# Kernel optimization log

Hardware: AMD Instinct MI355X
Metric: run time of the kernel (lower is better)

The kernel has to match this reference:

```python
import jax, jax.numpy as jnp
import numpy as np

START_ID = 1  # id of the start symbol in the vocabulary


def setup_inputs() -> dict:
    key = jax.random.key(0)
    ks = jax.random.split(key, 11)
    B, T, V, E, H, F = 64, 32, 10000, 300, 256, 4096
    s = 0.05
    return {
        "X": jax.random.normal(ks[0], (B, F), jnp.float32),
        "emb_table": jax.random.normal(ks[1], (V, E), jnp.float32),
        "fc1_w": jax.random.normal(ks[2], (H, F), jnp.float32) * s,
        "fc1_b": jax.random.normal(ks[3], (H,), jnp.float32) * s,
        "w_ih": jax.random.normal(ks[4], (4 * H, H + E), jnp.float32) * s,
        "w_hh": jax.random.normal(ks[5], (4 * H, H), jnp.float32) * s,
        "b_ih": jax.random.normal(ks[6], (4 * H,), jnp.float32) * s,
        "b_hh": jax.random.normal(ks[7], (4 * H,), jnp.float32) * s,
        "fc2_w": jax.random.normal(ks[8], (V, H), jnp.float32) * s,
        "fc2_b": jax.random.normal(ks[9], (V,), jnp.float32) * s,
        "label": jax.random.randint(ks[10], (T, B), 0, V, jnp.int64),
        "max_sentence_len": T,
    }


def reference(X, emb_table, fc1_w, fc1_b, w_ih, w_hh, b_ih, b_hh, fc2_w, fc2_b,
              label, max_sentence_len):
    T = max_sentence_len
    B = X.shape[0]
    V, H = fc2_w.shape
    E = emb_table.shape[1]

    # fc1: project image features to hidden size
    Xp = X @ fc1_w.T + fc1_b  # [B, H]

    # word embedding input per step: step 1 uses start symbol,
    # step idx>=2 uses teacher-forced embedding of label[idx-1]
    start_emb = jnp.broadcast_to(emb_table[START_ID], (1, B, E))
    tf_emb = emb_table[label[1:T - 1]]          # [T-2, B, E]
    embeds = jnp.concatenate([start_emb, tf_emb], axis=0)  # [T-1, B, E]

    h0 = jnp.zeros((B, H), X.dtype)
    c0 = jnp.zeros((B, H), X.dtype)

    def step(carry, e):
        h, c = carry
        x = jnp.concatenate([Xp, e], axis=1)  # [B, H+E]
        gates = x @ w_ih.T + b_ih + h @ w_hh.T + b_hh  # [B, 4H]
        i, f, g, o = jnp.split(gates, 4, axis=1)
        i = jax.nn.sigmoid(i)
        f = jax.nn.sigmoid(f)
        g = jnp.tanh(g)
        o = jax.nn.sigmoid(o)
        c = f * c + i * g
        h = o * jnp.tanh(c)
        logp = jax.nn.log_softmax(h @ fc2_w.T + fc2_b, axis=-1)  # [B, V]
        return (h, c), logp

    _, probs = jax.lax.scan(step, (h0, c0), embeds)  # [T-1, B, V]

    # first timestep: one-hot of the start word (as in the torch code)
    start_onehot = jnp.zeros((1, B, V), X.dtype).at[:, :, START_ID].set(1.0)
    result = jnp.concatenate([start_onehot, probs], axis=0)  # [T, B, V]
    return jnp.transpose(result, (1, 0, 2))  # [B, T, V]
```

## Files before the change

### kernel.cpp

```cpp
#include <hip/hip_runtime.h>
#include <hip/hip_bf16.h>
#include <math.h>

#define B_   64
#define T_   32
#define S_   31
#define V_   10000
#define E_   300
#define H_   256
#define F_   4096
#define G4   1024
#define HE   556
#define MPAD 2048
#define NPAD 10112
#define START_ID 1
#define NBL  4

#define FP0 10112
#define FP1 (FP0 + 128)
#define FP2 (FP1 + 2500)
#define FP3 (FP2 + 512)
#define FP4 (FP3 + 300)

typedef __bf16 bf16x8 __attribute__((ext_vector_type(8)));
typedef float  f32x4  __attribute__((ext_vector_type(4)));

__device__ __forceinline__ float bf16bits_to_f(unsigned int u) {
    union { unsigned int i; float f; } c; c.i = u; return c.f;
}
__device__ __forceinline__ unsigned short f_to_bf16bits(float f) {
    union { float f; unsigned int i; } c; c.f = f;
    unsigned int r = c.i + 0x7fffu + ((c.i >> 16) & 1);
    return (unsigned short)(r >> 16);
}
__device__ __forceinline__ float sigm(float x) { return 1.f / (1.f + __expf(-x)); }
__device__ __forceinline__ float tanh_fast(float x) { return 1.f - 2.f / (__expf(2.f * x) + 1.f); }

__global__ void k_front(const float* __restrict__ fc2_w,
                        __hip_bfloat16* __restrict__ fc2bf,
                        __hip_bfloat16* __restrict__ Hs,
                        const float* __restrict__ w_hh,
                        unsigned short* __restrict__ wpack,
                        float* __restrict__ out,
                        const float* __restrict__ X,
                        const float* __restrict__ fc1_w,
                        const float* __restrict__ fc1_b,
                        float* __restrict__ Xp_part,
                        const float* __restrict__ w_ih,
                        float* __restrict__ wie) {
    int bid = blockIdx.x, tid = threadIdx.x;
    if (bid < FP0) {
        size_t i = (size_t)bid * 256 + tid;
        float v = (i < (size_t)V_ * H_) ? fc2_w[i] : 0.f;
        fc2bf[i] = __float2bfloat16(v);
        if (i < (size_t)(MPAD - S_ * B_) * H_)
            Hs[(size_t)S_ * B_ * H_ + i] = __float2bfloat16(0.f);
    } else if (bid < FP1) {
        int t = (bid - FP0) * 256 + tid;
        int lane = t & 63, frag = t >> 6;
        int kf = frag & 7, nt = (frag >> 3) & 7, w = frag >> 6;
        int l16 = lane & 15, quad = lane >> 4;
        int j = (l16 & 3) * 256 + w * 32 + nt * 4 + (l16 >> 2);
        int k0 = kf * 32 + quad * 8;
        const float* src = w_hh + (size_t)j * H_ + k0;
        float4 a0 = *(const float4*)(src);
        float4 a1 = *(const float4*)(src + 4);
        unsigned short pk[8];
        pk[0] = f_to_bf16bits(a0.x); pk[1] = f_to_bf16bits(a0.y);
        pk[2] = f_to_bf16bits(a0.z); pk[3] = f_to_bf16bits(a0.w);
        pk[4] = f_to_bf16bits(a1.x); pk[5] = f_to_bf16bits(a1.y);
        pk[6] = f_to_bf16bits(a1.z); pk[7] = f_to_bf16bits(a1.w);
        uint4 st;
        st.x = (unsigned)pk[0] | ((unsigned)pk[1] << 16);
        st.y = (unsigned)pk[2] | ((unsigned)pk[3] << 16);
        st.z = (unsigned)pk[4] | ((unsigned)pk[5] << 16);
        st.w = (unsigned)pk[6] | ((unsigned)pk[7] << 16);
        *(uint4*)(wpack + (size_t)frag * 512 + lane * 8) = st;
    } else if (bid < FP2) {
        int i = (bid - FP1) * 256 + tid;
        if (i < B_ * V_) {
            int b = i / V_, v = i - b * V_;
            out[(size_t)b * T_ * V_ + v] = (v == START_ID) ? 1.f : 0.f;
        }
    } else if (bid < FP3) {
        __shared__ __align__(16) float xs[512];
        int r = bid - FP2;
        int b = r >> 3, q = r & 7;
        const float4* xrow = (const float4*)(X + (size_t)b * F_ + q * 512);
        if (tid < 128) ((float4*)xs)[tid] = xrow[tid];
        __syncthreads();
        int k = tid;
        const float4* w = (const float4*)(fc1_w + (size_t)k * F_ + q * 512);
        float acc = 0.f;
        #pragma unroll 8
        for (int f = 0; f < 128; ++f) {
            float4 wv = w[f];
            float4 xv = ((const float4*)xs)[f];
            acc += wv.x * xv.x + wv.y * xv.y + wv.z * xv.z + wv.w * xv.w;
        }
        if (q == 0) acc += fc1_b[k];
        Xp_part[((size_t)(q * 64 + b)) * 256 + k] = acc;
    } else if (bid < FP4) {
        int idx = (bid - FP3) * 256 + tid;
        int kk = idx >> 10, j = idx & 1023;
        float4 v = *(const float4*)(w_ih + (size_t)j * HE + H_ + kk * 4);
        ((float4*)wie)[(size_t)kk * 1024 + j] = v;
    }
}

__global__ void k_gconst(const float* __restrict__ Xp_part, const float* __restrict__ w_ih,
                         const float* __restrict__ b_ih, const float* __restrict__ b_hh,
                         float* __restrict__ gconst) {
    __shared__ __align__(16) float xs[H_];
    int b = blockIdx.x;
    float s = 0.f;
    #pragma unroll
    for (int q = 0; q < 8; ++q) s += Xp_part[((size_t)(q * 64 + b)) * 256 + threadIdx.x];
    xs[threadIdx.x] = s;
    __syncthreads();
    #pragma unroll
    for (int q = 0; q < 4; ++q) {
        int j = threadIdx.x + q * 256;
        const float* w = w_ih + (size_t)j * HE;
        float acc = 0.f;
        #pragma unroll 8
        for (int k = 0; k < H_ / 4; ++k) {
            float4 wv = *(const float4*)(w + k * 4);
            float4 xv = ((const float4*)xs)[k];
            acc += wv.x * xv.x + wv.y * xv.y + wv.z * xv.z + wv.w * xv.w;
        }
        gconst[b * G4 + j] = acc + b_ih[j] + b_hh[j];
    }
}

__global__ void k_ge(const float* __restrict__ emb, const int* __restrict__ label,
                     const float* __restrict__ wie, const float* __restrict__ gconst,
                     unsigned short* __restrict__ gfullT) {
    __shared__ __align__(16) float es[8][E_];
    int jt = blockIdx.x, bt = blockIdx.y, t = blockIdx.z;
    for (int i = threadIdx.x; i < 8 * E_; i += 256) {
        int b8 = i / E_, e = i - b8 * E_;
        int b = bt * 8 + b8;
        int idx = (t == 0) ? START_ID : label[t * B_ + b];
        es[b8][e] = emb[(size_t)idx * E_ + e];
    }
    __syncthreads();
    int j = jt * 256 + threadIdx.x;
    const float4* wp4 = (const float4*)wie + j;
    float acc[8] = {0.f, 0.f, 0.f, 0.f, 0.f, 0.f, 0.f, 0.f};
    for (int kk = 0; kk < E_ / 4; ++kk) {
        float4 wv = wp4[(size_t)kk * 1024];
        #pragma unroll
        for (int b8 = 0; b8 < 8; ++b8) {
            float4 ev = *(const float4*)(&es[b8][kk * 4]);
            acc[b8] += wv.x * ev.x + wv.y * ev.y + wv.z * ev.z + wv.w * ev.w;
        }
    }
    int u = threadIdx.x;
    int tile = u >> 2;
    int m = (u & 3) * 4 + jt;
    size_t base = ((((size_t)t * NBL + (bt >> 1)) * 64 + tile) * 16 + (bt & 1) * 8) * 16 + m;
    #pragma unroll
    for (int b8 = 0; b8 < 8; ++b8)
        gfullT[base + (size_t)b8 * 16] =
            f_to_bf16bits(acc[b8] + gconst[(bt * 8 + b8) * G4 + j]);
}

__global__ __launch_bounds__(512)
__attribute__((amdgpu_waves_per_eu(2, 2)))
void k_lstm(const unsigned short* __restrict__ gfullT,
            const unsigned short* __restrict__ wpack,
            __hip_bfloat16* __restrict__ Hs_) {
    unsigned short* Hs = (unsigned short*)Hs_;
    int bg = blockIdx.x;
    int tid = threadIdx.x;
    int w = tid >> 6, lane = tid & 63;
    int l16 = lane & 15, quad = lane >> 4;

    __shared__ __align__(16) unsigned short hs[16 * 264];
    __shared__ __align__(16) unsigned short blds[8 * 16 * 64 * 8];

    const unsigned short* wpb = wpack + (size_t)(w * 8) * 8 * 512 + lane * 8;
    bf16x8 wr0[8], wr1[8], wr2[8], wr3[8];
    #pragma unroll
    for (int kf = 0; kf < 8; ++kf) wr0[kf] = *(const bf16x8*)(wpb + (0 * 8 + kf) * 512);
    #pragma unroll
    for (int kf = 0; kf < 8; ++kf) wr1[kf] = *(const bf16x8*)(wpb + (1 * 8 + kf) * 512);
    #pragma unroll
    for (int kf = 0; kf < 8; ++kf) wr2[kf] = *(const bf16x8*)(wpb + (2 * 8 + kf) * 512);
    #pragma unroll
    for (int kf = 0; kf < 8; ++kf) wr3[kf] = *(const bf16x8*)(wpb + (3 * 8 + kf) * 512);

    #pragma unroll
    for (int f2 = 0; f2 < 16; ++f2) {
        int nt = 4 + (f2 >> 3), kf = f2 & 7;
        bf16x8 v = *(const bf16x8*)(wpb + (nt * 8 + kf) * 512);
        *(bf16x8*)(blds + ((size_t)(w * 16 + f2) * 64 + lane) * 8) = v;
    }

    for (int i = tid; i < 16 * 264 / 8; i += 512)
        ((uint4*)hs)[i] = make_uint4(0, 0, 0, 0);
    __syncthreads();

    float c[8] = {0.f, 0.f, 0.f, 0.f, 0.f, 0.f, 0.f, 0.f};
    const unsigned short* bl = blds + (size_t)(w * 16) * 512 + lane * 8;
    const unsigned short* hb = hs + l16 * 264 + quad * 8;
    int orow = tid >> 5, ocol = tid & 31;

    for (int t = 0; t < S_; ++t) {
        if (t > 0) {
            uint4 wv = *(const uint4*)(hs + orow * 264 + ocol * 8);
            *(uint4*)(Hs + ((size_t)((t - 1) * B_ + bg * 16 + orow)) * H_ + ocol * 8) = wv;
        }
        uint2 gf[8];
        const unsigned short* gtb = gfullT +
            ((((size_t)t * NBL + bg) * 64 + w * 8) * 256) + l16 * 16 + quad * 4;
        #pragma unroll
        for (int nt = 0; nt < 8; ++nt) gf[nt] = *(const uint2*)(gtb + nt * 256);
        bf16x8 hf[8];
        #pragma unroll
        for (int kf = 0; kf < 8; ++kf) hf[kf] = *(const bf16x8*)(hb + kf * 32);
        __syncthreads();

        bf16x8 s6[8];
        #pragma unroll
        for (int kf = 0; kf < 8; ++kf) s6[kf] = *(const bf16x8*)(wpb + (6 * 8 + kf) * 512);

#define DO_NT(nt, WSRC)                                                         \
        {                                                                       \
            f32x4 acc;                                                          \
            acc[0] = bf16bits_to_f(gf[nt].x << 16);                             \
            acc[1] = bf16bits_to_f(gf[nt].x & 0xffff0000u);                     \
            acc[2] = bf16bits_to_f(gf[nt].y << 16);                             \
            acc[3] = bf16bits_to_f(gf[nt].y & 0xffff0000u);                     \
            _Pragma("unroll")                                                   \
            for (int kf = 0; kf < 8; ++kf)                                      \
                acc = __builtin_amdgcn_mfma_f32_16x16x32_bf16(WSRC[kf], hf[kf], \
                                                              acc, 0, 0, 0);   \
            float ig = sigm(acc[0]);                                            \
            float fg = sigm(acc[1]);                                            \
            float gg = tanh_fast(acc[2]);                                       \
            float og = sigm(acc[3]);                                            \
            c[nt] = fg * c[nt] + ig * gg;                                       \
            float hv = og * tanh_fast(c[nt]);                                   \
            hs[l16 * 264 + w * 32 + (nt) * 4 + quad] = f_to_bf16bits(hv);       \
        }

        DO_NT(0, wr0)
        DO_NT(1, wr1)
        DO_NT(2, wr2)
        DO_NT(3, wr3)
        {
            bf16x8 w4[8];
            #pragma unroll
            for (int kf = 0; kf < 8; ++kf) w4[kf] = *(const bf16x8*)(bl + kf * 512);
            DO_NT(4, w4)
        }
        bf16x8 s7[8];
        #pragma unroll
        for (int kf = 0; kf < 8; ++kf) s7[kf] = *(const bf16x8*)(wpb + (7 * 8 + kf) * 512);
        {
            bf16x8 w5[8];
            #pragma unroll
            for (int kf = 0; kf < 8; ++kf) w5[kf] = *(const bf16x8*)(bl + (8 + kf) * 512);
            DO_NT(5, w5)
        }
        DO_NT(6, s6)
        DO_NT(7, s7)
#undef DO_NT
        __syncthreads();
    }
    {
        uint4 v = *(const uint4*)(hs + orow * 264 + ocol * 8);
        *(uint4*)(Hs + ((size_t)((S_ - 1) * B_ + bg * 16 + orow)) * H_ + ocol * 8) = v;
    }
}

__global__ __launch_bounds__(256) void k_gemm(const unsigned short* __restrict__ A,
                                              const unsigned short* __restrict__ Bw,
                                              const float* __restrict__ bias,
                                              float* __restrict__ out) {
    int nt = blockIdx.x, mt = blockIdx.y;
    int w = threadIdx.x >> 6, lane = threadIdx.x & 63;
    int l16 = lane & 15, quad = lane >> 4;
    int m0 = mt * 128 + (w >> 1) * 64;
    int n0 = nt * 128 + (w & 1) * 64;
    f32x4 acc[4][4] = {};
    const unsigned short* Ap = A + (size_t)(m0 + l16) * H_ + quad * 8;
    const unsigned short* Bp = Bw + (size_t)(n0 + l16) * H_ + quad * 8;
    #pragma unroll
    for (int k = 0; k < H_; k += 32) {
        bf16x8 a[4], bb[4];
        #pragma unroll
        for (int i = 0; i < 4; ++i) {
            a[i]  = *(const bf16x8*)(Ap + (size_t)i * 16 * H_ + k);
            bb[i] = *(const bf16x8*)(Bp + (size_t)i * 16 * H_ + k);
        }
        #pragma unroll
        for (int i = 0; i < 4; ++i)
            #pragma unroll
            for (int jn = 0; jn < 4; ++jn)
                acc[i][jn] = __builtin_amdgcn_mfma_f32_16x16x32_bf16(a[i], bb[jn], acc[i][jn], 0, 0, 0);
    }
    #pragma unroll
    for (int i = 0; i < 4; ++i) {
        #pragma unroll
        for (int jn = 0; jn < 4; ++jn) {
            #pragma unroll
            for (int r = 0; r < 4; ++r) {
                int m = m0 + i * 16 + quad * 4 + r;
                int n = n0 + jn * 16 + l16;
                if (m < S_ * B_ && n < V_) {
                    int t = m >> 6, b = m & 63;
                    out[((size_t)b * T_ + t + 1) * V_ + n] = acc[i][jn][r] + bias[n];
                }
            }
        }
    }
}

__global__ __launch_bounds__(256) void k_lsm(float* __restrict__ out) {
    __shared__ __align__(16) float rowbuf[V_];
    __shared__ float rmx[256], rsum[256];
    int m = blockIdx.x;
    int t = m >> 6, b = m & 63;
    float* row = out + ((size_t)b * T_ + t + 1) * V_;
    int tid = threadIdx.x;
    float mx = -1e30f, sum = 0.f;
    for (int v4 = tid; v4 < V_ / 4; v4 += 256) {
        float4 x = ((const float4*)row)[v4];
        ((float4*)rowbuf)[v4] = x;
        float m4 = fmaxf(fmaxf(x.x, x.y), fmaxf(x.z, x.w));
        if (m4 > mx) { sum *= __expf(mx - m4); mx = m4; }
        sum += __expf(x.x - mx) + __expf(x.y - mx) + __expf(x.z - mx) + __expf(x.w - mx);
    }
    rmx[tid] = mx; rsum[tid] = sum;
    __syncthreads();
    for (int s = 128; s > 0; s >>= 1) {
        if (tid < s) {
            float ma = rmx[tid], mb = rmx[tid + s];
            float sa = rsum[tid], sb = rsum[tid + s];
            float mm = fmaxf(ma, mb);
            rmx[tid] = mm;
            rsum[tid] = sa * __expf(ma - mm) + sb * __expf(mb - mm);
        }
        __syncthreads();
    }
    float lse = rmx[0] + logf(rsum[0]);
    for (int v4 = tid; v4 < V_ / 4; v4 += 256) {
        float4 x = ((const float4*)rowbuf)[v4];
        x.x -= lse; x.y -= lse; x.z -= lse; x.w -= lse;
        ((float4*)row)[v4] = x;
    }
}

extern "C" void kernel_launch(void* const* d_in, const int* in_sizes, int n_in,
                              void* d_out, int out_size, void* d_ws, size_t ws_size,
                              hipStream_t stream) {
    const float* X      = (const float*)d_in[0];
    const float* emb    = (const float*)d_in[1];
    const float* fc1_w  = (const float*)d_in[2];
    const float* fc1_b  = (const float*)d_in[3];
    const float* w_ih   = (const float*)d_in[4];
    const float* w_hh   = (const float*)d_in[5];
    const float* b_ih   = (const float*)d_in[6];
    const float* b_hh   = (const float*)d_in[7];
    const float* fc2_w  = (const float*)d_in[8];
    const float* fc2_b  = (const float*)d_in[9];
    const int*   label  = (const int*)d_in[10];
    float* out = (float*)d_out;

    char* ws = (char*)d_ws;
    float*          Xp_part = (float*)(ws);
    float*          gconst  = (float*)(ws + 524288);
    unsigned short* gfullT  = (unsigned short*)(ws + 786432);
    __hip_bfloat16* Hs      = (__hip_bfloat16*)(ws + 4849664);
    __hip_bfloat16* fc2bf   = (__hip_bfloat16*)(ws + 5898240);
    unsigned short* wpack   = (unsigned short*)(ws + 11075584);
    float*          wie     = (float*)(ws + 11599872);

    k_front <<<FP4, 256, 0, stream>>>(fc2_w, fc2bf, Hs, w_hh, wpack, out,
                                      X, fc1_w, fc1_b, Xp_part, w_ih, wie);
    k_gconst<<<B_, 256, 0, stream>>>(Xp_part, w_ih, b_ih, b_hh, gconst);
    k_ge    <<<dim3(4, 8, S_), 256, 0, stream>>>(emb, label, wie, gconst, gfullT);
    k_lstm  <<<NBL, 512, 0, stream>>>(gfullT, wpack, Hs);
    k_gemm  <<<dim3(NPAD / 128, MPAD / 128), 256, 0, stream>>>((const unsigned short*)Hs,
                                                              (const unsigned short*)fc2bf, fc2_b, out);
    k_lsm   <<<S_ * B_, 256, 0, stream>>>(out);
}
```

Measured before the change: 473.4 us.

## Double-buffer LSTM hidden state in LDS to drop a per-step barrier

Splits the shared hidden-state buffer into two ping-pong buffers, so each timestep reads h from one and writes the new h to the other. This removes the mid-step __syncthreads that separated reading h from overwriting it. It also starts the MFMA accumulation from zero and adds the precomputed input gates afterwards, so the global gate loads are off the MFMA dependency chain, and pins the register-resident weights with empty asm to stop rematerialisation. In exchange it doubles the LDS used for h and moves the s7 weight load later, which may expose its latency.

```diff
diff --git a/kernel.cpp b/kernel.cpp
--- a/kernel.cpp
+++ b/kernel.cpp
@@ -35,6 +35,13 @@
 }
 __device__ __forceinline__ float sigm(float x) { return 1.f / (1.f + __expf(-x)); }
 __device__ __forceinline__ float tanh_fast(float x) { return 1.f - 2.f / (__expf(2.f * x) + 1.f); }
+
+__device__ __forceinline__ void pinv(bf16x8 &v) {
+    union { bf16x8 b; unsigned int u[4]; } x;
+    x.b = v;
+    asm volatile("" : "+v"(x.u[0]), "+v"(x.u[1]), "+v"(x.u[2]), "+v"(x.u[3]));
+    v = x.b;
+}
 
 __global__ void k_front(const float* __restrict__ fc2_w,
                         __hip_bfloat16* __restrict__ fc2bf,
@@ -177,7 +184,8 @@
     int w = tid >> 6, lane = tid & 63;
     int l16 = lane & 15, quad = lane >> 4;
 
-    __shared__ __align__(16) unsigned short hs[16 * 264];
+    __shared__ __align__(16) unsigned short hs0[16 * 264];
+    __shared__ __align__(16) unsigned short hs1[16 * 264];
     __shared__ __align__(16) unsigned short blds[8 * 16 * 64 * 8];
 
     const unsigned short* wpb = wpack + (size_t)(w * 8) * 8 * 512 + lane * 8;
@@ -190,6 +198,10 @@
     for (int kf = 0; kf < 8; ++kf) wr2[kf] = *(const bf16x8*)(wpb + (2 * 8 + kf) * 512);
     #pragma unroll
     for (int kf = 0; kf < 8; ++kf) wr3[kf] = *(const bf16x8*)(wpb + (3 * 8 + kf) * 512);
+    #pragma unroll
+    for (int kf = 0; kf < 8; ++kf) {
+        pinv(wr0[kf]); pinv(wr1[kf]); pinv(wr2[kf]); pinv(wr3[kf]);
+    }
 
     #pragma unroll
     for (int f2 = 0; f2 < 16; ++f2) {
@@ -199,17 +211,24 @@
     }
 
     for (int i = tid; i < 16 * 264 / 8; i += 512)
-        ((uint4*)hs)[i] = make_uint4(0, 0, 0, 0);
+        ((uint4*)hs0)[i] = make_uint4(0, 0, 0, 0);
     __syncthreads();
 
     float c[8] = {0.f, 0.f, 0.f, 0.f, 0.f, 0.f, 0.f, 0.f};
     const unsigned short* bl = blds + (size_t)(w * 16) * 512 + lane * 8;
-    const unsigned short* hb = hs + l16 * 264 + quad * 8;
     int orow = tid >> 5, ocol = tid & 31;
 
     for (int t = 0; t < S_; ++t) {
+        unsigned short* hcur = (t & 1) ? hs1 : hs0;
+        unsigned short* hnxt = (t & 1) ? hs0 : hs1;
+
+        const unsigned short* hb = hcur + l16 * 264 + quad * 8;
+        bf16x8 hf[8];
+        #pragma unroll
+        for (int kf = 0; kf < 8; ++kf) hf[kf] = *(const bf16x8*)(hb + kf * 32);
+
         if (t > 0) {
-            uint4 wv = *(const uint4*)(hs + orow * 264 + ocol * 8);
+            uint4 wv = *(const uint4*)(hcur + orow * 264 + ocol * 8);
             *(uint4*)(Hs + ((size_t)((t - 1) * B_ + bg * 16 + orow)) * H_ + ocol * 8) = wv;
         }
         uint2 gf[8];
@@ -217,33 +236,28 @@
             ((((size_t)t * NBL + bg) * 64 + w * 8) * 256) + l16 * 16 + quad * 4;
         #pragma unroll
         for (int nt = 0; nt < 8; ++nt) gf[nt] = *(const uint2*)(gtb + nt * 256);
-        bf16x8 hf[8];
-        #pragma unroll
-        for (int kf = 0; kf < 8; ++kf) hf[kf] = *(const bf16x8*)(hb + kf * 32);
-        __syncthreads();
-
         bf16x8 s6[8];
         #pragma unroll
         for (int kf = 0; kf < 8; ++kf) s6[kf] = *(const bf16x8*)(wpb + (6 * 8 + kf) * 512);
 
 #define DO_NT(nt, WSRC)                                                         \
         {                                                                       \
-            f32x4 acc;                                                          \
-            acc[0] = bf16bits_to_f(gf[nt].x << 16);                             \
-            acc[1] = bf16bits_to_f(gf[nt].x & 0xffff0000u);                     \
-            acc[2] = bf16bits_to_f(gf[nt].y << 16);                             \
-            acc[3] = bf16bits_to_f(gf[nt].y & 0xffff0000u);                     \
+            f32x4 acc = {0.f, 0.f, 0.f, 0.f};                                   \
             _Pragma("unroll")                                                   \
             for (int kf = 0; kf < 8; ++kf)                                      \
                 acc = __builtin_amdgcn_mfma_f32_16x16x32_bf16(WSRC[kf], hf[kf], \
                                                               acc, 0, 0, 0);   \
-            float ig = sigm(acc[0]);                                            \
-            float fg = sigm(acc[1]);                                            \
-            float gg = tanh_fast(acc[2]);                                       \
-            float og = sigm(acc[3]);                                            \
+            float g0 = acc[0] + bf16bits_to_f(gf[nt].x << 16);                  \
+            float g1 = acc[1] + bf16bits_to_f(gf[nt].x & 0xffff0000u);          \
+            float g2 = acc[2] + bf16bits_to_f(gf[nt].y << 16);                  \
+            float g3 = acc[3] + bf16bits_to_f(gf[nt].y & 0xffff0000u);          \
+            float ig = sigm(g0);                                                \
+            float fg = sigm(g1);                                                \
+            float gg = tanh_fast(g2);                                           \
+            float og = sigm(g3);                                                \
             c[nt] = fg * c[nt] + ig * gg;                                       \
             float hv = og * tanh_fast(c[nt]);                                   \
-            hs[l16 * 264 + w * 32 + (nt) * 4 + quad] = f_to_bf16bits(hv);       \
+            hnxt[l16 * 264 + w * 32 + (nt) * 4 + quad] = f_to_bf16bits(hv);     \
         }
 
         DO_NT(0, wr0)
@@ -256,9 +270,6 @@
             for (int kf = 0; kf < 8; ++kf) w4[kf] = *(const bf16x8*)(bl + kf * 512);
             DO_NT(4, w4)
         }
-        bf16x8 s7[8];
-        #pragma unroll
-        for (int kf = 0; kf < 8; ++kf) s7[kf] = *(const bf16x8*)(wpb + (7 * 8 + kf) * 512);
         {
             bf16x8 w5[8];
             #pragma unroll
@@ -266,12 +277,17 @@
             DO_NT(5, w5)
         }
         DO_NT(6, s6)
-        DO_NT(7, s7)
+        {
+            bf16x8 s7[8];
+            #pragma unroll
+            for (int kf = 0; kf < 8; ++kf) s7[kf] = *(const bf16x8*)(wpb + (7 * 8 + kf) * 512);
+            DO_NT(7, s7)
+        }
 #undef DO_NT
         __syncthreads();
     }
     {
-        uint4 v = *(const uint4*)(hs + orow * 264 + ocol * 8);
+        uint4 v = *(const uint4*)(hs1 + orow * 264 + ocol * 8);
         *(uint4*)(Hs + ((size_t)((S_ - 1) * B_ + bg * 16 + orow)) * H_ + ocol * 8) = v;
     }
 }
```

Measured after the change: 508.5 us. 1.07x slower.

## Double-buffer LSTM hidden state in LDS and prefetch next step's gate inputs

Applied to the files above, without the earlier changes.

The recurrent LSTM kernel now keeps two shared-memory hidden-state buffers and alternates between them, so each timestep needs one barrier instead of two. It also loads the precomputed input-gate values for step t+1 into registers while step t computes, which hides global-load latency. The cost is extra LDS use and more live registers for the second gate buffer. That could raise register pressure on a kernel already pinned to two waves per EU.

```diff
diff --git a/kernel.cpp b/kernel.cpp
--- a/kernel.cpp
+++ b/kernel.cpp
@@ -177,19 +177,20 @@
     int w = tid >> 6, lane = tid & 63;
     int l16 = lane & 15, quad = lane >> 4;
 
-    __shared__ __align__(16) unsigned short hs[16 * 264];
+    __shared__ __align__(16) unsigned short hs0[16 * 264];
+    __shared__ __align__(16) unsigned short hs1[16 * 264];
     __shared__ __align__(16) unsigned short blds[8 * 16 * 64 * 8];
 
     const unsigned short* wpb = wpack + (size_t)(w * 8) * 8 * 512 + lane * 8;
+
     bf16x8 wr0[8], wr1[8], wr2[8], wr3[8];
     #pragma unroll
-    for (int kf = 0; kf < 8; ++kf) wr0[kf] = *(const bf16x8*)(wpb + (0 * 8 + kf) * 512);
-    #pragma unroll
-    for (int kf = 0; kf < 8; ++kf) wr1[kf] = *(const bf16x8*)(wpb + (1 * 8 + kf) * 512);
-    #pragma unroll
-    for (int kf = 0; kf < 8; ++kf) wr2[kf] = *(const bf16x8*)(wpb + (2 * 8 + kf) * 512);
-    #pragma unroll
-    for (int kf = 0; kf < 8; ++kf) wr3[kf] = *(const bf16x8*)(wpb + (3 * 8 + kf) * 512);
+    for (int kf = 0; kf < 8; ++kf) {
+        wr0[kf] = *(const bf16x8*)(wpb + (0 * 8 + kf) * 512);
+        wr1[kf] = *(const bf16x8*)(wpb + (1 * 8 + kf) * 512);
+        wr2[kf] = *(const bf16x8*)(wpb + (2 * 8 + kf) * 512);
+        wr3[kf] = *(const bf16x8*)(wpb + (3 * 8 + kf) * 512);
+    }
 
     #pragma unroll
     for (int f2 = 0; f2 < 16; ++f2) {
@@ -199,40 +200,26 @@
     }
 
     for (int i = tid; i < 16 * 264 / 8; i += 512)
-        ((uint4*)hs)[i] = make_uint4(0, 0, 0, 0);
+        ((uint4*)hs0)[i] = make_uint4(0, 0, 0, 0);
     __syncthreads();
 
     float c[8] = {0.f, 0.f, 0.f, 0.f, 0.f, 0.f, 0.f, 0.f};
     const unsigned short* bl = blds + (size_t)(w * 16) * 512 + lane * 8;
-    const unsigned short* hb = hs + l16 * 264 + quad * 8;
     int orow = tid >> 5, ocol = tid & 31;
-
-    for (int t = 0; t < S_; ++t) {
-        if (t > 0) {
-            uint4 wv = *(const uint4*)(hs + orow * 264 + ocol * 8);
-            *(uint4*)(Hs + ((size_t)((t - 1) * B_ + bg * 16 + orow)) * H_ + ocol * 8) = wv;
-        }
-        uint2 gf[8];
-        const unsigned short* gtb = gfullT +
-            ((((size_t)t * NBL + bg) * 64 + w * 8) * 256) + l16 * 16 + quad * 4;
-        #pragma unroll
-        for (int nt = 0; nt < 8; ++nt) gf[nt] = *(const uint2*)(gtb + nt * 256);
-        bf16x8 hf[8];
-        #pragma unroll
-        for (int kf = 0; kf < 8; ++kf) hf[kf] = *(const bf16x8*)(hb + kf * 32);
-        __syncthreads();
-
-        bf16x8 s6[8];
-        #pragma unroll
-        for (int kf = 0; kf < 8; ++kf) s6[kf] = *(const bf16x8*)(wpb + (6 * 8 + kf) * 512);
-
-#define DO_NT(nt, WSRC)                                                         \
+    const unsigned short* gbase = gfullT + ((size_t)bg * 64 + w * 8) * 256
+                                  + l16 * 16 + quad * 4;
+
+    uint2 gfA[8], gfB[8];
+    #pragma unroll
+    for (int nt = 0; nt < 8; ++nt) gfA[nt] = *(const uint2*)(gbase + nt * 256);
+
+#define DO_NT(nt, WSRC, GF, HNXT)                                               \
         {                                                                       \
             f32x4 acc;                                                          \
-            acc[0] = bf16bits_to_f(gf[nt].x << 16);                             \
-            acc[1] = bf16bits_to_f(gf[nt].x & 0xffff0000u);                     \
-            acc[2] = bf16bits_to_f(gf[nt].y << 16);                             \
-            acc[3] = bf16bits_to_f(gf[nt].y & 0xffff0000u);                     \
+            acc[0] = bf16bits_to_f((GF)[nt].x << 16);                           \
+            acc[1] = bf16bits_to_f((GF)[nt].x & 0xffff0000u);                   \
+            acc[2] = bf16bits_to_f((GF)[nt].y << 16);                           \
+            acc[3] = bf16bits_to_f((GF)[nt].y & 0xffff0000u);                   \
             _Pragma("unroll")                                                   \
             for (int kf = 0; kf < 8; ++kf)                                      \
                 acc = __builtin_amdgcn_mfma_f32_16x16x32_bf16(WSRC[kf], hf[kf], \
@@ -243,35 +230,67 @@
             float og = sigm(acc[3]);                                            \
             c[nt] = fg * c[nt] + ig * gg;                                       \
             float hv = og * tanh_fast(c[nt]);                                   \
-            hs[l16 * 264 + w * 32 + (nt) * 4 + quad] = f_to_bf16bits(hv);       \
-        }
-
-        DO_NT(0, wr0)
-        DO_NT(1, wr1)
-        DO_NT(2, wr2)
-        DO_NT(3, wr3)
-        {
-            bf16x8 w4[8];
-            #pragma unroll
-            for (int kf = 0; kf < 8; ++kf) w4[kf] = *(const bf16x8*)(bl + kf * 512);
-            DO_NT(4, w4)
-        }
-        bf16x8 s7[8];
-        #pragma unroll
-        for (int kf = 0; kf < 8; ++kf) s7[kf] = *(const bf16x8*)(wpb + (7 * 8 + kf) * 512);
-        {
-            bf16x8 w5[8];
-            #pragma unroll
-            for (int kf = 0; kf < 8; ++kf) w5[kf] = *(const bf16x8*)(bl + (8 + kf) * 512);
-            DO_NT(5, w5)
-        }
-        DO_NT(6, s6)
-        DO_NT(7, s7)
+            (HNXT)[l16 * 264 + w * 32 + (nt) * 4 + quad] = f_to_bf16bits(hv);   \
+        }
+
+#define LSTM_STEP(T, HCUR, HNXT, GFC, GFN, WRITEPREV)                           \
+    {                                                                           \
+        const unsigned short* hb = (HCUR) + l16 * 264 + quad * 8;               \
+        bf16x8 hf[8];                                                           \
+        _Pragma("unroll")                                                       \
+        for (int kf = 0; kf < 8; ++kf) hf[kf] = *(const bf16x8*)(hb + kf * 32); \
+        if (WRITEPREV) {                                                        \
+            uint4 wv = *(const uint4*)((HCUR) + orow * 264 + ocol * 8);         \
+            *(uint4*)(Hs + ((size_t)(((T) - 1) * B_ + bg * 16 + orow)) * H_     \
+                      + ocol * 8) = wv;                                         \
+        }                                                                       \
+        if ((T) + 1 < S_) {                                                     \
+            const unsigned short* gtn = gbase +                                 \
+                (size_t)((T) + 1) * (NBL * 64 * 256);                           \
+            _Pragma("unroll")                                                   \
+            for (int nt = 0; nt < 8; ++nt)                                      \
+                (GFN)[nt] = *(const uint2*)(gtn + nt * 256);                    \
+        }                                                                       \
+        bf16x8 s6[8];                                                           \
+        _Pragma("unroll")                                                       \
+        for (int kf = 0; kf < 8; ++kf)                                          \
+            s6[kf] = *(const bf16x8*)(wpb + (6 * 8 + kf) * 512);                \
+        DO_NT(0, wr0, GFC, HNXT)                                                \
+        DO_NT(1, wr1, GFC, HNXT)                                                \
+        DO_NT(2, wr2, GFC, HNXT)                                                \
+        DO_NT(3, wr3, GFC, HNXT)                                                \
+        {                                                                       \
+            bf16x8 w4[8];                                                       \
+            _Pragma("unroll")                                                   \
+            for (int kf = 0; kf < 8; ++kf)                                      \
+                w4[kf] = *(const bf16x8*)(bl + kf * 512);                       \
+            DO_NT(4, w4, GFC, HNXT)                                             \
+        }                                                                       \
+        bf16x8 s7[8];                                                           \
+        _Pragma("unroll")                                                       \
+        for (int kf = 0; kf < 8; ++kf)                                          \
+            s7[kf] = *(const bf16x8*)(wpb + (7 * 8 + kf) * 512);                \
+        {                                                                       \
+            bf16x8 w5[8];                                                       \
+            _Pragma("unroll")                                                   \
+            for (int kf = 0; kf < 8; ++kf)                                      \
+                w5[kf] = *(const bf16x8*)(bl + (8 + kf) * 512);                 \
+            DO_NT(5, w5, GFC, HNXT)                                             \
+        }                                                                       \
+        DO_NT(6, s6, GFC, HNXT)                                                 \
+        DO_NT(7, s7, GFC, HNXT)                                                 \
+        __syncthreads();                                                        \
+    }
+
+    for (int t = 0; t < S_ - 1; t += 2) {
+        LSTM_STEP(t,     hs0, hs1, gfA, gfB, (t > 0));
+        LSTM_STEP(t + 1, hs1, hs0, gfB, gfA, true);
+    }
+    LSTM_STEP(S_ - 1, hs0, hs1, gfA, gfB, true);
+#undef LSTM_STEP
 #undef DO_NT
-        __syncthreads();
-    }
     {
-        uint4 v = *(const uint4*)(hs + orow * 264 + ocol * 8);
+        uint4 v = *(const uint4*)(hs1 + orow * 264 + ocol * 8);
         *(uint4*)(Hs + ((size_t)((S_ - 1) * B_ + bg * 16 + orow)) * H_ + ocol * 8) = v;
     }
 }
```

New measurement: 523.3 us. +10.5%, slower.
